# Optimization experiments

Measured on AMD Instinct MI355X. Metric: run time of the kernel, lower is better.

Reference implementation:

```python
import jax, jax.numpy as jnp
import numpy as np

B, N = 128, 1369
DINO, CLIP, H = 384, 512, 8
D = CLIP // H  # head_dim = 64
EPS = 1e-5


def setup_inputs() -> dict:
    key = jax.random.key(0)
    ks = jax.random.split(key, 8)
    s_clip = 1.0 / np.sqrt(CLIP)
    s_dino = 1.0 / np.sqrt(DINO)
    return {
        "dino_features": jax.random.normal(ks[0], (B, N, DINO), jnp.float32),
        "clip_features": jax.random.normal(ks[1], (B, CLIP), jnp.float32),
        "Wq": jax.random.uniform(ks[2], (CLIP, CLIP), jnp.float32, -s_clip, s_clip),
        "bq": jnp.zeros((CLIP,), jnp.float32),
        "Wk": jax.random.uniform(ks[3], (DINO, CLIP), jnp.float32, -s_dino, s_dino),
        "bk": jnp.zeros((CLIP,), jnp.float32),
        "Wv": jax.random.uniform(ks[4], (DINO, CLIP), jnp.float32, -s_dino, s_dino),
        "bv": jnp.zeros((CLIP,), jnp.float32),
        "temperature": jnp.ones((1,), jnp.float32),
        "ln_gamma": jnp.ones((CLIP,), jnp.float32),
        "ln_beta": jnp.zeros((CLIP,), jnp.float32),
    }


def reference(dino_features, clip_features, Wq, bq, Wk, bk, Wv, bv,
              temperature, ln_gamma, ln_beta):
    # Q: (B, H, D) -- single query token from CLIP
    Q = (clip_features @ Wq + bq).reshape(B, H, D)
    # K, V: (B, N, H, D)
    K = (dino_features @ Wk + bk).reshape(B, N, H, D)
    V = (dino_features @ Wv + bv).reshape(B, N, H, D)
    scale = jnp.sqrt(jnp.float32(D)) * temperature[0]
    # attention logits over patches: (B, H, N)
    logits = jnp.einsum("bhd,bnhd->bhn", Q, K) / scale
    attn = jax.nn.softmax(logits, axis=-1)  # dropout is identity in eval mode
    out = jnp.einsum("bhn,bnhd->bhd", attn, V).reshape(B, CLIP)
    # LayerNorm over last dim
    mu = out.mean(axis=-1, keepdims=True)
    var = out.var(axis=-1, keepdims=True)
    return (out - mu) * jax.lax.rsqrt(var + EPS) * ln_gamma + ln_beta
```

## Files before the change

kernel.cpp:

```cpp
#include <hip/hip_runtime.h>
#include <math.h>
#include <stdint.h>

#define B_    128
#define N_    1369
#define DINO_ 384
#define CLIP_ 512
#define H_    8
#define CHUNKS 8
#define CH     172
#define TROWS  12
#define SEGS   18
#define SMP    52

__device__ __forceinline__ float wave_sum(float v) {
  v += __shfl_xor(v, 1);  v += __shfl_xor(v, 2);  v += __shfl_xor(v, 4);
  v += __shfl_xor(v, 8);  v += __shfl_xor(v, 16); v += __shfl_xor(v, 32);
  return v;
}

__device__ __forceinline__ void gld16(const float* g, float* lds_base) {
  __builtin_amdgcn_global_load_lds(
      (const __attribute__((address_space(1))) void*)g,
      (__attribute__((address_space(3))) void*)lds_base, 16, 0, 0);
}

__global__ __launch_bounds__(256) void kqq(const float* __restrict__ clip,
                                           const float* __restrict__ Wq,
                                           const float* __restrict__ bq,
                                           const float* __restrict__ Wk,
                                           const float* __restrict__ temp,
                                           float* __restrict__ qkout) {
  const int b = blockIdx.x, tid = threadIdx.x;
  __shared__ float cl[CLIP_], qs[CLIP_];
  cl[tid] = clip[b * CLIP_ + tid];
  cl[tid + 256] = clip[b * CLIP_ + tid + 256];
  __syncthreads();
  #pragma unroll
  for (int half = 0; half < 2; ++half) {
    const int cc = tid + 256 * half;
    float acc = bq[cc];
    #pragma unroll 8
    for (int j = 0; j < CLIP_; ++j) acc += cl[j] * Wq[j * CLIP_ + cc];
    qs[cc] = acc;
  }
  __syncthreads();
  const float rs = 1.0f / (8.0f * temp[0]);
  #pragma unroll 1
  for (int r = 0; r < 12; ++r) {
    const int e = tid + 256 * r;
    const int h = e / DINO_;
    const int j = e - h * DINO_;
    const float* wrow = Wk + (size_t)j * CLIP_ + h * 64;
    const float* qrow = qs + h * 64;
    float a0 = 0.f, a1 = 0.f, a2 = 0.f, a3 = 0.f;
    #pragma unroll
    for (int d = 0; d < 64; d += 4) {
      const float4 wv = *(const float4*)(wrow + d);
      const float4 qv = *(const float4*)(qrow + d);
      a0 += wv.x * qv.x;  a1 += wv.y * qv.y;
      a2 += wv.z * qv.z;  a3 += wv.w * qv.w;
    }
    qkout[(size_t)b * 3072 + e] = ((a0 + a1) + (a2 + a3)) * rs;
  }
}

__global__ __launch_bounds__(256, 4) void kmain(const float* __restrict__ dino,
                                                const float* __restrict__ qk,
                                                float* __restrict__ ps,
                                                float* __restrict__ pl) {
  __shared__ float lds[2 * TROWS * DINO_];
  __shared__ float lm[2][H_];

  const int blk = blockIdx.x;
  const int b = blk >> 3;
  const int c = blk & 7;
  const int n0 = c * CH;
  const int n1 = min(N_, n0 + CH);
  const int tid = threadIdx.x, w = tid >> 6, lane = tid & 63;
  const int m = lane & 31;
  const int G = lane >> 5;
  const int b4 = (lane >> 4) & 1, b3 = (lane >> 3) & 1;
  const int hO = 2 * b4 + b3;

  float qr[4][12];
  {
    const float* qb = qk + (size_t)b * 3072 + (G * 4) * DINO_ + 4 * m;
    #pragma unroll
    for (int j = 0; j < 4; ++j)
      #pragma unroll
      for (int t = 0; t < 3; ++t) {
        const float4 v = *(const float4*)(qb + j * DINO_ + 128 * t);
        qr[j][4*t] = v.x; qr[j][4*t+1] = v.y; qr[j][4*t+2] = v.z; qr[j][4*t+3] = v.w;
      }
  }
  float s[4][12];
  #pragma unroll
  for (int j = 0; j < 4; ++j)
    #pragma unroll
    for (int q = 0; q < 12; ++q) s[j][q] = 0.0f;
  float l = 0.0f;

  const float* gdino = dino + (size_t)b * N_ * DINO_;
  const float* gclamp = dino + ((size_t)B_ * N_ * DINO_ - 4);
  const int ntiles = (n1 - n0 + TROWS - 1) / TROWS;

  {
    const float* gb = gdino + (size_t)n0 * DINO_;
    for (int sg = w; sg < SEGS; sg += 4) {
      const float* g = gb + sg * 256 + 4 * lane;
      if (g > gclamp) g = gclamp;
      gld16(g, lds + sg * 256);
    }
  }
  __syncthreads();

  for (int t = 0; t < ntiles; ++t) {
    float* cur = lds + ((t & 1) ? TROWS * DINO_ : 0);
    float* nxt = lds + ((t & 1) ? 0 : TROWS * DINO_);
    if (t + 1 < ntiles) {
      const float* gb = gdino + (size_t)(n0 + (t + 1) * TROWS) * DINO_;
      for (int sg = w; sg < SEGS; sg += 4) {
        const float* g = gb + sg * 256 + 4 * lane;
        if (g > gclamp) g = gclamp;
        gld16(g, nxt + sg * 256);
      }
    }
    const int tb = n0 + t * TROWS;
    #pragma unroll 1
    for (int k = 0; k < 3; ++k) {
      const int slot = w + 4 * k;
      if (tb + slot >= n1) break;
      const float* xr = cur + slot * DINO_ + 4 * m;
      const float4 x0 = *(const float4*)(xr);
      const float4 x1 = *(const float4*)(xr + 128);
      const float4 x2 = *(const float4*)(xr + 256);
      const float xv[12] = {x0.x, x0.y, x0.z, x0.w,
                            x1.x, x1.y, x1.z, x1.w,
                            x2.x, x2.y, x2.z, x2.w};
      float va[4];
      #pragma unroll
      for (int j = 0; j < 4; ++j) {
        float a = 0.f, bacc = 0.f;
        #pragma unroll
        for (int q = 0; q < 12; q += 2) {
          a    += qr[j][q]     * xv[q];
          bacc += qr[j][q + 1] * xv[q + 1];
        }
        va[j] = a + bacc;
      }
      float c0, c1;
      {
        const float t0 = __shfl_xor(va[0], 16), t1 = __shfl_xor(va[1], 16);
        const float t2 = __shfl_xor(va[2], 16), t3 = __shfl_xor(va[3], 16);
        c0 = b4 ? va[2] + t2 : va[0] + t0;
        c1 = b4 ? va[3] + t3 : va[1] + t1;
      }
      float d;
      {
        const float u0 = __shfl_xor(c0, 8), u1 = __shfl_xor(c1, 8);
        d = b3 ? c1 + u1 : c0 + u0;
      }
      d += __shfl_xor(d, 4);
      d += __shfl_xor(d, 2);
      d += __shfl_xor(d, 1);
      const float p = __expf(d);
      l += p;
      float P[4];
      P[0] = p;
      P[1] = __shfl_xor(p, 8);
      P[2] = __shfl_xor(p, 16);
      P[3] = __shfl_xor(P[1], 16);
      #pragma unroll
      for (int j = 0; j < 4; ++j)
        #pragma unroll
        for (int q = 0; q < 12; ++q) s[j][q] += P[j] * xv[q];
    }
    __syncthreads();
  }

  float* sm0 = lds;
  float* sm1 = lds + 64 * SMP;
  if (w >= 2) {
    float* dst = (w == 2 ? sm0 : sm1) + lane * SMP;
    #pragma unroll
    for (int j = 0; j < 4; ++j)
      #pragma unroll
      for (int t = 0; t < 3; ++t)
        *(float4*)(dst + j * 12 + 4 * t) =
            make_float4(s[j][4*t], s[j][4*t+1], s[j][4*t+2], s[j][4*t+3]);
    if ((lane & 7) == 0) lm[w - 2][4 * G + hO] = l;
  }
  __syncthreads();
  if (w < 2) {
    const float* src = (w == 0 ? sm0 : sm1) + lane * SMP;
    #pragma unroll
    for (int j = 0; j < 4; ++j)
      #pragma unroll
      for (int t = 0; t < 3; ++t) {
        const float4 v = *(const float4*)(src + j * 12 + 4 * t);
        s[j][4*t] += v.x; s[j][4*t+1] += v.y; s[j][4*t+2] += v.z; s[j][4*t+3] += v.w;
      }
    l += lm[w][4 * G + hO];
  }
  __syncthreads();
  if (w == 1) {
    float* dst = sm0 + lane * SMP;
    #pragma unroll
    for (int j = 0; j < 4; ++j)
      #pragma unroll
      for (int t = 0; t < 3; ++t)
        *(float4*)(dst + j * 12 + 4 * t) =
            make_float4(s[j][4*t], s[j][4*t+1], s[j][4*t+2], s[j][4*t+3]);
    if ((lane & 7) == 0) lm[0][4 * G + hO] = l;
  }
  __syncthreads();
  if (w == 0) {
    const float* src = sm0 + lane * SMP;
    #pragma unroll
    for (int j = 0; j < 4; ++j)
      #pragma unroll
      for (int t = 0; t < 3; ++t) {
        const float4 v = *(const float4*)(src + j * 12 + 4 * t);
        s[j][4*t] += v.x; s[j][4*t+1] += v.y; s[j][4*t+2] += v.z; s[j][4*t+3] += v.w;
      }
    l += lm[0][4 * G + hO];
    float* pso = ps + (size_t)blk * 3072;
    #pragma unroll
    for (int j = 0; j < 4; ++j) {
      const int h = 4 * G + (hO ^ j);
      float* o = pso + h * DINO_ + 4 * m;
      #pragma unroll
      for (int t = 0; t < 3; ++t)
        *(float4*)(o + 128 * t) =
            make_float4(s[j][4*t], s[j][4*t+1], s[j][4*t+2], s[j][4*t+3]);
    }
    if ((lane & 7) == 0) pl[blk * H_ + 4 * G + hO] = l;
  }
}

__global__ __launch_bounds__(512) void kmf(const float* __restrict__ ps,
                                           const float* __restrict__ pl,
                                           const float* __restrict__ Wv,
                                           const float* __restrict__ bv,
                                           const float* __restrict__ gamma,
                                           const float* __restrict__ beta,
                                           float* __restrict__ out) {
  const int b = blockIdx.x, tid = threadIdx.x;
  __shared__ float sfl[3072];
  __shared__ float rL[H_];
  float a[6];
  #pragma unroll
  for (int r = 0; r < 6; ++r) {
    const int e = tid + 512 * r;
    float acc = 0.0f;
    #pragma unroll
    for (int cc = 0; cc < CHUNKS; ++cc)
      acc += ps[(size_t)(b * CHUNKS + cc) * 3072 + e];
    a[r] = acc;
  }
  if (tid < H_) {
    float L = 0.0f;
    #pragma unroll
    for (int cc = 0; cc < CHUNKS; ++cc) L += pl[(b * CHUNKS + cc) * H_ + tid];
    rL[tid] = 1.0f / L;
  }
  __syncthreads();
  #pragma unroll
  for (int r = 0; r < 6; ++r) {
    const int e = tid + 512 * r;
    sfl[e] = a[r] * rL[e / DINO_];
  }
  __syncthreads();
  const int w = tid >> 6, lane = tid & 63;
  const float* srow = sfl + (tid >> 6) * DINO_;
  float acc = bv[tid];
  #pragma unroll 8
  for (int d = 0; d < DINO_; ++d) acc += srow[d] * Wv[d * CLIP_ + tid];
  float sum = wave_sum(acc);
  float sq  = wave_sum(acc * acc);
  __shared__ float rS[8], rQ[8];
  if (lane == 0) { rS[w] = sum; rQ[w] = sq; }
  __syncthreads();
  float tot = 0.0f, totq = 0.0f;
  #pragma unroll
  for (int i = 0; i < 8; ++i) { tot += rS[i]; totq += rQ[i]; }
  const float mu = tot * (1.0f / 512.0f);
  const float var = totq * (1.0f / 512.0f) - mu * mu;
  const float rstd = rsqrtf(var + 1e-5f);
  out[(size_t)b * CLIP_ + tid] = (acc - mu) * rstd * gamma[tid] + beta[tid];
}

extern "C" void kernel_launch(void* const* d_in, const int* in_sizes, int n_in,
                              void* d_out, int out_size, void* d_ws, size_t ws_size,
                              hipStream_t stream) {
  const float* dino  = (const float*)d_in[0];
  const float* clip  = (const float*)d_in[1];
  const float* Wq    = (const float*)d_in[2];
  const float* bq    = (const float*)d_in[3];
  const float* Wk    = (const float*)d_in[4];
  const float* Wv    = (const float*)d_in[6];
  const float* bv    = (const float*)d_in[7];
  const float* temp  = (const float*)d_in[8];
  const float* gamma = (const float*)d_in[9];
  const float* beta  = (const float*)d_in[10];
  float* out = (float*)d_out;

  float* ws  = (float*)d_ws;
  float* qkb = ws;
  float* ps  = qkb + 393216;
  float* pl  = ps  + 3145728;

  kqq  <<<B_,           256, 0, stream>>>(clip, Wq, bq, Wk, temp, qkb);
  kmain<<<B_ * CHUNKS,  256, 0, stream>>>(dino, qkb, ps, pl);
  kmf  <<<B_,           512, 0, stream>>>(ps, pl, Wv, bv, gamma, beta, out);
}
```

Measured before the change: 511.4 us.

## Use a 4-deep per-wave LDS prefetch ring and split the Q/QK precompute kernels

The main kernel's double-buffered tile loop, which needed a block-wide barrier every tile, becomes a 4-slot ring of 8-row tiles. Each wave loads exactly the LDS segments it later reads and waits on vmcnt, so no barrier is needed inside the loop. Chunks per batch go from 8 to 6 and occupancy hints change. The fused Q and Q·Wk^T precompute is split into two kernels with 2D grids to expose more blocks. The risks are lower occupancy from the larger LDS footprint and relying on exact per-wave vmcnt accounting for correctness.

```diff
diff --git a/kernel.cpp b/kernel.cpp
--- a/kernel.cpp
+++ b/kernel.cpp
@@ -7,10 +7,11 @@
 #define DINO_ 384
 #define CLIP_ 512
 #define H_    8
-#define CHUNKS 8
-#define CH     172
-#define TROWS  12
-#define SEGS   18
+#define CHUNKS 6
+#define CH     229
+#define TROWS  8
+#define DEPTH  4
+#define SEGW   3
 #define SMP    52
 
 __device__ __forceinline__ float wave_sum(float v) {
@@ -25,56 +26,58 @@
       (__attribute__((address_space(3))) void*)lds_base, 16, 0, 0);
 }
 
-__global__ __launch_bounds__(256) void kqq(const float* __restrict__ clip,
-                                           const float* __restrict__ Wq,
-                                           const float* __restrict__ bq,
-                                           const float* __restrict__ Wk,
+__global__ __launch_bounds__(256) void kq(const float* __restrict__ clip,
+                                          const float* __restrict__ Wq,
+                                          const float* __restrict__ bq,
+                                          float* __restrict__ Q) {
+  const int b = blockIdx.x;
+  const int c = blockIdx.y * 256 + threadIdx.x;
+  __shared__ float cl[CLIP_];
+  cl[threadIdx.x] = clip[b * CLIP_ + threadIdx.x];
+  cl[threadIdx.x + 256] = clip[b * CLIP_ + threadIdx.x + 256];
+  __syncthreads();
+  float acc = bq[c];
+  #pragma unroll 8
+  for (int j = 0; j < CLIP_; ++j) acc += cl[j] * Wq[j * CLIP_ + c];
+  Q[b * CLIP_ + c] = acc;
+}
+
+__global__ __launch_bounds__(256) void kqk(const float* __restrict__ Wk,
+                                           const float* __restrict__ Q,
                                            const float* __restrict__ temp,
                                            float* __restrict__ qkout) {
-  const int b = blockIdx.x, tid = threadIdx.x;
-  __shared__ float cl[CLIP_], qs[CLIP_];
-  cl[tid] = clip[b * CLIP_ + tid];
-  cl[tid + 256] = clip[b * CLIP_ + tid + 256];
-  __syncthreads();
-  #pragma unroll
-  for (int half = 0; half < 2; ++half) {
-    const int cc = tid + 256 * half;
-    float acc = bq[cc];
-    #pragma unroll 8
-    for (int j = 0; j < CLIP_; ++j) acc += cl[j] * Wq[j * CLIP_ + cc];
-    qs[cc] = acc;
-  }
-  __syncthreads();
+  const int b = blockIdx.x;
+  const int e = blockIdx.y * 256 + threadIdx.x;
+  __shared__ float qs[CLIP_];
+  qs[threadIdx.x] = Q[b * CLIP_ + threadIdx.x];
+  qs[threadIdx.x + 256] = Q[b * CLIP_ + threadIdx.x + 256];
+  __syncthreads();
+  const int h = e / DINO_;
+  const int j = e - h * DINO_;
   const float rs = 1.0f / (8.0f * temp[0]);
-  #pragma unroll 1
-  for (int r = 0; r < 12; ++r) {
-    const int e = tid + 256 * r;
-    const int h = e / DINO_;
-    const int j = e - h * DINO_;
-    const float* wrow = Wk + (size_t)j * CLIP_ + h * 64;
-    const float* qrow = qs + h * 64;
-    float a0 = 0.f, a1 = 0.f, a2 = 0.f, a3 = 0.f;
-    #pragma unroll
-    for (int d = 0; d < 64; d += 4) {
-      const float4 wv = *(const float4*)(wrow + d);
-      const float4 qv = *(const float4*)(qrow + d);
-      a0 += wv.x * qv.x;  a1 += wv.y * qv.y;
-      a2 += wv.z * qv.z;  a3 += wv.w * qv.w;
-    }
-    qkout[(size_t)b * 3072 + e] = ((a0 + a1) + (a2 + a3)) * rs;
-  }
-}
-
-__global__ __launch_bounds__(256, 4) void kmain(const float* __restrict__ dino,
+  const float* wrow = Wk + (size_t)j * CLIP_ + h * 64;
+  const float* qrow = qs + h * 64;
+  float a0 = 0.f, a1 = 0.f, a2 = 0.f, a3 = 0.f;
+  #pragma unroll
+  for (int d = 0; d < 64; d += 4) {
+    const float4 wv = *(const float4*)(wrow + d);
+    const float4 qv = *(const float4*)(qrow + d);
+    a0 += wv.x * qv.x;  a1 += wv.y * qv.y;
+    a2 += wv.z * qv.z;  a3 += wv.w * qv.w;
+  }
+  qkout[(size_t)b * 3072 + e] = ((a0 + a1) + (a2 + a3)) * rs;
+}
+
+__global__ __launch_bounds__(256, 3) void kmain(const float* __restrict__ dino,
                                                 const float* __restrict__ qk,
                                                 float* __restrict__ ps,
                                                 float* __restrict__ pl) {
-  __shared__ float lds[2 * TROWS * DINO_];
+  __shared__ float lds[DEPTH * TROWS * DINO_];
   __shared__ float lm[2][H_];
 
   const int blk = blockIdx.x;
-  const int b = blk >> 3;
-  const int c = blk & 7;
+  const int b = blk / CHUNKS;
+  const int c = blk - b * CHUNKS;
   const int n0 = c * CH;
   const int n1 = min(N_, n0 + CH);
   const int tid = threadIdx.x, w = tid >> 6, lane = tid & 63;
@@ -94,6 +97,8 @@
         qr[j][4*t] = v.x; qr[j][4*t+1] = v.y; qr[j][4*t+2] = v.z; qr[j][4*t+3] = v.w;
       }
   }
+  asm volatile("s_waitcnt vmcnt(0)" ::: "memory");
+
   float s[4][12];
   #pragma unroll
   for (int j = 0; j < 4; ++j)
@@ -105,79 +110,89 @@
   const float* gclamp = dino + ((size_t)B_ * N_ * DINO_ - 4);
   const int ntiles = (n1 - n0 + TROWS - 1) / TROWS;
 
-  {
-    const float* gb = gdino + (size_t)n0 * DINO_;
-    for (int sg = w; sg < SEGS; sg += 4) {
+  #pragma unroll
+  for (int pt = 0; pt < 3; ++pt) {
+    const float* gb = gdino + (size_t)(n0 + pt * TROWS) * DINO_;
+    float* buf = lds + pt * (TROWS * DINO_);
+    #pragma unroll
+    for (int j = 0; j < SEGW; ++j) {
+      const int sg = SEGW * w + j;
       const float* g = gb + sg * 256 + 4 * lane;
       if (g > gclamp) g = gclamp;
-      gld16(g, lds + sg * 256);
+      gld16(g, buf + sg * 256);
     }
   }
-  __syncthreads();
 
   for (int t = 0; t < ntiles; ++t) {
-    float* cur = lds + ((t & 1) ? TROWS * DINO_ : 0);
-    float* nxt = lds + ((t & 1) ? 0 : TROWS * DINO_);
-    if (t + 1 < ntiles) {
-      const float* gb = gdino + (size_t)(n0 + (t + 1) * TROWS) * DINO_;
-      for (int sg = w; sg < SEGS; sg += 4) {
+    asm volatile("s_waitcnt vmcnt(6)" ::: "memory");
+    __builtin_amdgcn_sched_barrier(0);
+    {
+      const float* gb = gdino + (size_t)(n0 + (t + 3) * TROWS) * DINO_;
+      float* buf = lds + ((t + 3) & 3) * (TROWS * DINO_);
+      #pragma unroll
+      for (int j = 0; j < SEGW; ++j) {
+        const int sg = SEGW * w + j;
         const float* g = gb + sg * 256 + 4 * lane;
         if (g > gclamp) g = gclamp;
-        gld16(g, nxt + sg * 256);
+        gld16(g, buf + sg * 256);
       }
     }
+    const float* cur = lds + (t & 3) * (TROWS * DINO_);
     const int tb = n0 + t * TROWS;
-    #pragma unroll 1
-    for (int k = 0; k < 3; ++k) {
-      const int slot = w + 4 * k;
-      if (tb + slot >= n1) break;
-      const float* xr = cur + slot * DINO_ + 4 * m;
-      const float4 x0 = *(const float4*)(xr);
-      const float4 x1 = *(const float4*)(xr + 128);
-      const float4 x2 = *(const float4*)(xr + 256);
-      const float xv[12] = {x0.x, x0.y, x0.z, x0.w,
-                            x1.x, x1.y, x1.z, x1.w,
-                            x2.x, x2.y, x2.z, x2.w};
-      float va[4];
-      #pragma unroll
-      for (int j = 0; j < 4; ++j) {
-        float a = 0.f, bacc = 0.f;
+    #pragma unroll
+    for (int k = 0; k < 2; ++k) {
+      const int slot = 2 * w + k;
+      if (tb + slot < n1) {
+        const float* xr = cur + slot * DINO_ + 4 * m;
+        const float4 x0 = *(const float4*)(xr);
+        const float4 x1 = *(const float4*)(xr + 128);
+        const float4 x2 = *(const float4*)(xr + 256);
+        const float xv[12] = {x0.x, x0.y, x0.z, x0.w,
+                              x1.x, x1.y, x1.z, x1.w,
+                              x2.x, x2.y, x2.z, x2.w};
+        float va[4];
         #pragma unroll
-        for (int q = 0; q < 12; q += 2) {
-          a    += qr[j][q]     * xv[q];
-          bacc += qr[j][q + 1] * xv[q + 1];
+        for (int j = 0; j < 4; ++j) {
+          float a = 0.f, bacc = 0.f;
+          #pragma unroll
+          for (int q = 0; q < 12; q += 2) {
+            a    += qr[j][q]     * xv[q];
+            bacc += qr[j][q + 1] * xv[q + 1];
+          }
+          va[j] = a + bacc;
         }
-        va[j] = a + bacc;
-      }
-      float c0, c1;
-      {
-        const float t0 = __shfl_xor(va[0], 16), t1 = __shfl_xor(va[1], 16);
-        const float t2 = __shfl_xor(va[2], 16), t3 = __shfl_xor(va[3], 16);
-        c0 = b4 ? va[2] + t2 : va[0] + t0;
-        c1 = b4 ? va[3] + t3 : va[1] + t1;
-      }
-      float d;
-      {
-        const float u0 = __shfl_xor(c0, 8), u1 = __shfl_xor(c1, 8);
-        d = b3 ? c1 + u1 : c0 + u0;
-      }
-      d += __shfl_xor(d, 4);
-      d += __shfl_xor(d, 2);
-      d += __shfl_xor(d, 1);
-      const float p = __expf(d);
-      l += p;
-      float P[4];
-      P[0] = p;
-      P[1] = __shfl_xor(p, 8);
-      P[2] = __shfl_xor(p, 16);
-      P[3] = __shfl_xor(P[1], 16);
-      #pragma unroll
-      for (int j = 0; j < 4; ++j)
+        float c0, c1;
+        {
+          const float t0 = __shfl_xor(va[0], 16), t1 = __shfl_xor(va[1], 16);
+          const float t2 = __shfl_xor(va[2], 16), t3 = __shfl_xor(va[3], 16);
+          c0 = b4 ? va[2] + t2 : va[0] + t0;
+          c1 = b4 ? va[3] + t3 : va[1] + t1;
+        }
+        float d;
+        {
+          const float u0 = __shfl_xor(c0, 8), u1 = __shfl_xor(c1, 8);
+          d = b3 ? c1 + u1 : c0 + u0;
+        }
+        d += __shfl_xor(d, 4);
+        d += __shfl_xor(d, 2);
+        d += __shfl_xor(d, 1);
+        const float p = __expf(d);
+        l += p;
+        float P[4];
+        P[0] = p;
+        P[1] = __shfl_xor(p, 8);
+        P[2] = __shfl_xor(p, 16);
+        P[3] = __shfl_xor(P[1], 16);
         #pragma unroll
-        for (int q = 0; q < 12; ++q) s[j][q] += P[j] * xv[q];
+        for (int j = 0; j < 4; ++j)
+          #pragma unroll
+          for (int q = 0; q < 12; ++q) s[j][q] += P[j] * xv[q];
+      }
     }
-    __syncthreads();
-  }
+  }
+
+  asm volatile("s_waitcnt vmcnt(0)" ::: "memory");
+  __syncthreads();
 
   float* sm0 = lds;
   float* sm1 = lds + 64 * SMP;
@@ -307,11 +322,13 @@
   float* out = (float*)d_out;
 
   float* ws  = (float*)d_ws;
-  float* qkb = ws;
+  float* Q   = ws;
+  float* qkb = Q   + 65536;
   float* ps  = qkb + 393216;
-  float* pl  = ps  + 3145728;
-
-  kqq  <<<B_,           256, 0, stream>>>(clip, Wq, bq, Wk, temp, qkb);
+  float* pl  = ps  + 2359296;
+
+  kq   <<<dim3(B_, 2),  256, 0, stream>>>(clip, Wq, bq, Q);
+  kqk  <<<dim3(B_, 12), 256, 0, stream>>>(Wk, Q, temp, qkb);
   kmain<<<B_ * CHUNKS,  256, 0, stream>>>(dino, qkb, ps, pl);
   kmf  <<<B_,           512, 0, stream>>>(ps, pl, Wv, bv, gamma, beta, out);
 }
```

Measured after the change: 470.6 us. 8.0% less time.
